# Kernel tuning notes

Hardware: AMD Instinct MI355X
Metric: run time of the kernel (lower is better)

The kernel has to match this reference:

```python
import jax, jax.numpy as jnp
import numpy as np

B, M, N, D, H = 8, 64, 64, 256, 8

def setup_inputs() -> dict:
    key = jax.random.key(0)
    kx, kq, kk, kv, ko = jax.random.split(key, 5)
    x = jax.random.normal(kx, (B, M, N, D), dtype=jnp.float32)
    q = jax.random.normal(kq, (H, D, D), dtype=jnp.float32)
    k = jax.random.normal(kk, (D, D), dtype=jnp.float32)
    v = jax.random.normal(kv, (D, D), dtype=jnp.float32)
    o = jax.random.normal(ko, (H, D, D), dtype=jnp.float32)
    return {"x": x, "q": q, "k": k, "v": v, "o": o}

def reference(x, q, k, v, o):
    # x: [b,m,n,d]; q,o: [h,d,d]; k,v: [d,d]
    Q = jnp.einsum('bmnd,hdk->bhmnk', x, q)      # [b,h,m,n,d]
    h_half = Q.shape[1] // 2
    Q1, Q2 = Q[:, :h_half], Q[:, h_half:]
    K = jnp.einsum('bmnd,dk->bmnk', x, k)        # [b,m,n,d]
    V = jnp.einsum('bmnd,dv->bmnv', x, v)        # [b,m,n,d]

    # Axis 1: attend along the m (row) axis for each column y
    logits1 = jnp.einsum('bhxyk,bzyk->bhyxz', Q1, K)   # [b,h/2,n,m,m]
    scores1 = jax.nn.softmax(logits1, axis=-1)
    O1 = jnp.einsum('bhyxz,bzyv->bhxyv', scores1, V)   # [b,h/2,m,n,d]

    # Axis 2: attend along the n (column) axis for each row x
    logits2 = jnp.einsum('bhxyk,bxzk->bhxyz', Q2, K)   # [b,h/2,m,n,n]
    scores2 = jax.nn.softmax(logits2, axis=-1)
    O2 = jnp.einsum('bhxyz,bxzv->bhxyv', scores2, V)   # [b,h/2,m,n,d]

    O = jnp.concatenate([O1, O2], axis=1)              # [b,h,m,n,d]
    # Faithful to original: 'bhmnd,hdv->bmnd' keeps d, sums over h and v
    Z = jnp.einsum('bhmnd,hdv->bmnd', O, o)
    return Z
```

## Files before the change

kernel.cpp:

```cpp
#include <hip/hip_runtime.h>

typedef unsigned short u16;
typedef __attribute__((ext_vector_type(8))) short short8;
typedef __attribute__((ext_vector_type(4))) float f32x4;

__device__ __forceinline__ float bf2f(u16 u){ return __uint_as_float(((unsigned)u)<<16); }
__device__ __forceinline__ u16 f2bf(float f){
  unsigned u = __float_as_uint(f);
  unsigned r = u + 0x7fffu + ((u>>16)&1u);
  return (u16)(r>>16);
}

#define MFMA16(a,b,c) __builtin_amdgcn_mfma_f32_16x16x32_bf16(a,b,c,0,0,0)

static constexpr int XS_STR  = 264;
static constexpr int PS_STR  = 72;
static constexpr int WT_STR  = 72;
static constexpr int XHI_OFF = 0;
static constexpr int XLO_OFF = 16896;
static constexpr int GT_OFF  = 33792;
static constexpr int XVT_OFF = 50688;
static constexpr int PS_OFF  = 69120;
static constexpr int SMRE_OFF= 73728;
static constexpr int SMEM_BYTES = (73728 + 512)*2;

static constexpr int MH_SMEM = 70656*2;


__global__ void prep_kernel(const float* __restrict__ k, const float* __restrict__ v,
                            const float* __restrict__ o, u16* __restrict__ khi,
                            u16* __restrict__ klo, u16* __restrict__ vT,
                            float* __restrict__ soP){
  __shared__ float Ts[64*65];
  const int blk = blockIdx.x, tid = threadIdx.x;
  if (blk < 64){
    int base = blk*1024 + tid*4;
    const float4 f4 = *(const float4*)(k + base);
    ushort4 hv, lv;
    hv.x=f2bf(f4.x); lv.x=f2bf(f4.x-bf2f(hv.x));
    hv.y=f2bf(f4.y); lv.y=f2bf(f4.y-bf2f(hv.y));
    hv.z=f2bf(f4.z); lv.z=f2bf(f4.z-bf2f(hv.z));
    hv.w=f2bf(f4.w); lv.w=f2bf(f4.w-bf2f(hv.w));
    *(ushort4*)&khi[base] = hv;
    *(ushort4*)&klo[base] = lv;
  } else if (blk < 80){
    int t = blk - 64;
    const int bi = (t>>2)<<6, bj = (t&3)<<6;
    #pragma unroll
    for (int p=0;p<4;p++){
      int idx4 = tid + (p<<8);
      int i = idx4 >> 4, c4 = (idx4 & 15) << 2;
      const float4 f4 = *(const float4*)(v + ((bi+i)<<8) + bj + c4);
      Ts[i*65+c4]=f4.x; Ts[i*65+c4+1]=f4.y; Ts[i*65+c4+2]=f4.z; Ts[i*65+c4+3]=f4.w;
    }
    __syncthreads();
    #pragma unroll
    for (int p=0;p<2;p++){
      int ch = tid + (p<<8);
      int j = ch >> 3, i8 = (ch & 7) << 3;
      short8 t8;
      #pragma unroll
      for (int e=0;e<8;e++) t8[e] = (short)f2bf(Ts[(i8+e)*65 + j]);
      *(short8*)&vT[((bj+j)<<8) + bi + i8] = t8;
    }
  } else {
    int p = blk - 80;
    int h = p >> 5, base = (p & 31) << 3;
    int w = tid >> 6, l = tid & 63;
    #pragma unroll
    for (int i=0;i<2;i++){
      int row = base + w*2 + i;
      const float4 f4 = *(const float4*)(o + (((h<<8)+row)<<8) + (l<<2));
      float s = f4.x + f4.y + f4.z + f4.w;
      #pragma unroll
      for (int off=32; off>=1; off>>=1) s += __shfl_xor(s, off, 64);
      if (l==0) soP[(h<<8)+row] = s;
    }
  }
}

__global__ __launch_bounds__(256,1) void mh_kernel(
    const float* __restrict__ q, const u16* __restrict__ khi,
    const u16* __restrict__ klo, u16* __restrict__ mhi, u16* __restrict__ mlo)
{
  extern __shared__ u16 sm[];
  u16* Qhi = sm;
  u16* Qlo = sm + 16896;
  u16* Chi = sm + 33792;
  u16* Clo = sm + 52224;

  const int tid = threadIdx.x;
  const int w = tid >> 6, lane = tid & 63;
  const int quad = lane >> 4, m16 = lane & 15;
  const int cw = w << 6, koq = quad << 3;
  const int h = blockIdx.x >> 2, dt = (blockIdx.x & 3) << 6;

  #pragma unroll
  for (int i=0;i<16;i++){
    int idx4 = i*256 + tid;
    int tr = idx4 >> 6, c4 = (idx4 & 63) << 2;
    const float4 xv = *(const float4*)(q + (((h<<8)+dt+tr)<<8) + c4);
    ushort4 hv, lv;
    hv.x=f2bf(xv.x); lv.x=f2bf(xv.x-bf2f(hv.x));
    hv.y=f2bf(xv.y); lv.y=f2bf(xv.y-bf2f(hv.y));
    hv.z=f2bf(xv.z); lv.z=f2bf(xv.z-bf2f(hv.z));
    hv.w=f2bf(xv.w); lv.w=f2bf(xv.w-bf2f(hv.w));
    *(ushort4*)&Qhi[tr*XS_STR + c4] = hv;
    *(ushort4*)&Qlo[tr*XS_STR + c4] = lv;
  }
  __syncthreads();

  const f32x4 zf = {0.f,0.f,0.f,0.f};
  f32x4 acc[4][4];
  #pragma unroll
  for (int r=0;r<4;r++)
    #pragma unroll
    for (int c=0;c<4;c++) acc[r][c] = zf;

  short8 Bh[2][4], Bl[2][4];
  #pragma unroll
  for (int c=0;c<4;c++){
    Bh[0][c] = *(const short8*)&khi[(cw + c*16 + m16)*256 + koq];
    Bl[0][c] = *(const short8*)&klo[(cw + c*16 + m16)*256 + koq];
  }
  #pragma unroll
  for (int kk=0;kk<8;kk++){
    const int cur = kk&1, nxt = cur^1;
    if (kk<7){
      const int ko2 = ((kk+1)<<5) + koq;
      #pragma unroll
      for (int c=0;c<4;c++){
        Bh[nxt][c] = *(const short8*)&khi[(cw + c*16 + m16)*256 + ko2];
        Bl[nxt][c] = *(const short8*)&klo[(cw + c*16 + m16)*256 + ko2];
      }
    }
    const int ko = (kk<<5) + koq;
    short8 Ah[4], Al[4];
    #pragma unroll
    for (int r=0;r<4;r++) Ah[r] = *(const short8*)&Qhi[(r*16+m16)*XS_STR + ko];
    #pragma unroll
    for (int r=0;r<4;r++) Al[r] = *(const short8*)&Qlo[(r*16+m16)*XS_STR + ko];
    #pragma unroll
    for (int r=0;r<4;r++)
      #pragma unroll
      for (int c=0;c<4;c++){
        acc[r][c] = MFMA16(Ah[r], Bh[cur][c], acc[r][c]);
        acc[r][c] = MFMA16(Ah[r], Bl[cur][c], acc[r][c]);
        acc[r][c] = MFMA16(Al[r], Bh[cur][c], acc[r][c]);
      }
  }

  #pragma unroll
  for (int r=0;r<4;r++)
    #pragma unroll
    for (int c=0;c<4;c++)
      #pragma unroll
      for (int g=0; g<4; g++){
        int drow = r*16 + quad*4 + g;
        int dp   = cw + c*16 + m16;
        float vv = acc[r][c][g];
        u16 hh = f2bf(vv);
        Chi[dp*WT_STR + drow] = hh;
        Clo[dp*WT_STR + drow] = f2bf(vv - bf2f(hh));
      }
  __syncthreads();

  #pragma unroll
  for (int p=0;p<8;p++){
    int ch = tid + (p<<8);
    int dp = ch >> 3, i8 = (ch & 7) << 3;
    *(int4*)&mhi[(((h<<8)+dp)<<8) + dt + i8] = *(const int4*)&Chi[dp*WT_STR + i8];
    *(int4*)&mlo[(((h<<8)+dp)<<8) + dt + i8] = *(const int4*)&Clo[dp*WT_STR + i8];
  }
}

__global__ __launch_bounds__(512,2) void attn_kernel(
    const float* __restrict__ x, const u16* __restrict__ mhiP,
    const u16* __restrict__ mloP, const u16* __restrict__ vT,
    const float* __restrict__ soP, float* __restrict__ out)
{
  extern __shared__ u16 sm[];
  u16* Xhi = sm + XHI_OFF;
  u16* Xlo = sm + XLO_OFF;
  u16* Gt  = sm + GT_OFF;
  u16* Xvt = sm + XVT_OFF;
  u16* Ps  = sm + PS_OFF;
  float* SMf = (float*)(sm + SMRE_OFF);

  const int tid  = threadIdx.x;
  const int w    = tid >> 6, lane = tid & 63;
  const int quad = lane >> 4, m16 = lane & 15;
  const int br   = blockIdx.x >> 9;
  const int idx  = blockIdx.x & 511;
  const int b    = idx >> 6, s = idx & 63;
  const int cw   = w << 5;
  const int rs   = (w >> 1) << 4;
  const int zh   = w & 1;
  const int koq  = quad << 3;

  auto tok = [&](int t)->int {
    int m = br ? s : t;
    int n = br ? t : s;
    return (((b<<6) + m) << 14) + (n << 8);
  };

  #pragma unroll
  for (int i=0;i<8;i++){
    int idx4 = i*512 + tid;
    int tr = idx4 >> 6, c4 = (idx4 & 63) << 2;
    const float4 xv = *(const float4*)(x + tok(tr) + c4);
    ushort4 hv, lv;
    hv.x=f2bf(xv.x); lv.x=f2bf(xv.x-bf2f(hv.x));
    hv.y=f2bf(xv.y); lv.y=f2bf(xv.y-bf2f(hv.y));
    hv.z=f2bf(xv.z); lv.z=f2bf(xv.z-bf2f(hv.z));
    hv.w=f2bf(xv.w); lv.w=f2bf(xv.w-bf2f(hv.w));
    *(ushort4*)&Xhi[tr*XS_STR + c4] = hv;
    *(ushort4*)&Xlo[tr*XS_STR + c4] = lv;
  }
  __syncthreads();

  const f32x4 zf = {0.f,0.f,0.f,0.f};
  f32x4 acc[4][2];

  auto mm3 = [&](const u16* __restrict__ Whi, const u16* __restrict__ Wlo){
    #pragma unroll
    for (int r=0;r<4;r++){ acc[r][0] = zf; acc[r][1] = zf; }
    short8 Bh[2][2], Bl[2][2];
    #pragma unroll
    for (int c=0;c<2;c++){
      Bh[0][c] = *(const short8*)&Whi[(cw + c*16 + m16)*256 + koq];
      Bl[0][c] = *(const short8*)&Wlo[(cw + c*16 + m16)*256 + koq];
    }
    #pragma unroll
    for (int kk=0;kk<8;kk++){
      const int cur = kk&1, nxt = cur^1;
      if (kk<7){
        const int ko2 = ((kk+1)<<5) + koq;
        #pragma unroll
        for (int c=0;c<2;c++){
          Bh[nxt][c] = *(const short8*)&Whi[(cw + c*16 + m16)*256 + ko2];
          Bl[nxt][c] = *(const short8*)&Wlo[(cw + c*16 + m16)*256 + ko2];
        }
      }
      const int ko = (kk<<5) + koq;
      short8 Ah[4], Al[4];
      #pragma unroll
      for (int r=0;r<4;r++) Ah[r] = *(const short8*)&Xhi[(r*16+m16)*XS_STR + ko];
      #pragma unroll
      for (int r=0;r<4;r++) Al[r] = *(const short8*)&Xlo[(r*16+m16)*XS_STR + ko];
      #pragma unroll
      for (int r=0;r<4;r++)
        #pragma unroll
        for (int c=0;c<2;c++){
          acc[r][c] = MFMA16(Ah[r], Bh[cur][c], acc[r][c]);
          acc[r][c] = MFMA16(Ah[r], Bl[cur][c], acc[r][c]);
          acc[r][c] = MFMA16(Al[r], Bh[cur][c], acc[r][c]);
        }
    }
  };

  {
    #pragma unroll
    for (int r=0;r<4;r++){ acc[r][0] = zf; acc[r][1] = zf; }
    #pragma unroll
    for (int kk=0;kk<8;kk++){
      const int ko = (kk<<5) + koq;
      short8 A[4], Bf[2];
      #pragma unroll
      for (int r=0;r<4;r++) A[r]  = *(const short8*)&Xhi[(r*16+m16)*XS_STR + ko];
      #pragma unroll
      for (int c=0;c<2;c++) Bf[c] = *(const short8*)&vT[(cw + c*16 + m16)*256 + ko];
      #pragma unroll
      for (int r=0;r<4;r++)
        #pragma unroll
        for (int c=0;c<2;c++) acc[r][c] = MFMA16(A[r], Bf[c], acc[r][c]);
    }
    #pragma unroll
    for (int r=0;r<4;r++)
      #pragma unroll
      for (int c=0;c<2;c++)
        #pragma unroll
        for (int g=0; g<4; g++){
          int z  = r*16 + quad*4 + g;
          int vc = cw + c*16 + m16;
          Xvt[vc*WT_STR + z] = f2bf(acc[r][c][g]);
        }
  }

  f32x4 Z[4][2];
  #pragma unroll
  for (int r=0;r<4;r++){ Z[r][0] = zf; Z[r][1] = zf; }

  for (int h=0; h<4; h++){
    const int gh = br*4 + h;

    mm3(mhiP + gh*65536, mloP + gh*65536);
    #pragma unroll
    for (int r=0;r<4;r++)
      #pragma unroll
      for (int c=0;c<2;c++)
        #pragma unroll
        for (int g=0; g<4; g++){
          int row = r*16 + quad*4 + g;
          int col = cw + c*16 + m16;
          Gt[row*XS_STR + col] = f2bf(acc[r][c][g]);
        }
    __syncthreads();

    f32x4 L[2];
    L[0] = zf; L[1] = zf;
    #pragma unroll
    for (int kk=0;kk<8;kk++){
      const int ko = (kk<<5) + koq;
      short8 A = *(const short8*)&Gt[(rs+m16)*XS_STR + ko];
      #pragma unroll
      for (int c=0;c<2;c++)
        L[c] = MFMA16(A, *(const short8*)&Xhi[((zh<<5) + c*16+m16)*XS_STR + ko], L[c]);
      #pragma unroll
      for (int c=0;c<2;c++)
        L[c] = MFMA16(A, *(const short8*)&Xlo[((zh<<5) + c*16+m16)*XS_STR + ko], L[c]);
    }
    __syncthreads();
    #pragma unroll
    for (int r=0;r<4;r++)
      #pragma unroll
      for (int c=0;c<2;c++)
        #pragma unroll
        for (int g=0; g<4; g++){
          int row = r*16 + quad*4 + g;
          int col = cw + c*16 + m16;
          float vv = acc[r][c][g];
          u16 hh = f2bf(vv);
          Gt[row*XS_STR + col] = f2bf(vv - bf2f(hh));
        }
    __syncthreads();

    #pragma unroll
    for (int kk=0;kk<8;kk++){
      const int ko = (kk<<5) + koq;
      short8 A = *(const short8*)&Gt[(rs+m16)*XS_STR + ko];
      #pragma unroll
      for (int c=0;c<2;c++)
        L[c] = MFMA16(A, *(const short8*)&Xhi[((zh<<5) + c*16+m16)*XS_STR + ko], L[c]);
    }

    float mxl[4], sml[4];
    #pragma unroll
    for (int g=0; g<4; g++){
      float mx = fmaxf(L[0][g], L[1][g]);
      #pragma unroll
      for (int off=1; off<16; off<<=1) mx = fmaxf(mx, __shfl_xor(mx, off, 64));
      float sum = 0.f;
      #pragma unroll
      for (int c=0;c<2;c++){ float e = __expf(L[c][g]-mx); L[c][g] = e; sum += e; }
      #pragma unroll
      for (int off=1; off<16; off<<=1) sum += __shfl_xor(sum, off, 64);
      mxl[g] = mx; sml[g] = sum;
      if (m16 == 0){
        int row = rs + quad*4 + g;
        SMf[row*4 + zh*2]     = mx;
        SMf[row*4 + zh*2 + 1] = sum;
      }
    }
    __syncthreads();
    #pragma unroll
    for (int g=0; g<4; g++){
      int row = rs + quad*4 + g;
      float mxo = SMf[row*4 + (zh^1)*2];
      float smo = SMf[row*4 + (zh^1)*2 + 1];
      float M   = fmaxf(mxl[g], mxo);
      float al  = __expf(mxl[g]-M), ao = __expf(mxo-M);
      float scale = al / (sml[g]*al + smo*ao);
      #pragma unroll
      for (int c=0;c<2;c++)
        Ps[row*PS_STR + (zh<<5) + c*16 + m16] = f2bf(L[c][g]*scale);
    }
    __syncthreads();

    #pragma unroll
    for (int r=0;r<4;r++){ acc[r][0] = zf; acc[r][1] = zf; }
    #pragma unroll
    for (int kk=0;kk<2;kk++){
      const int ko = (kk<<5) + koq;
      short8 A[4], Bf[2];
      #pragma unroll
      for (int r=0;r<4;r++) A[r]  = *(const short8*)&Ps[(r*16+m16)*PS_STR + ko];
      #pragma unroll
      for (int c=0;c<2;c++) Bf[c] = *(const short8*)&Xvt[(cw + c*16 + m16)*WT_STR + ko];
      #pragma unroll
      for (int r=0;r<4;r++)
        #pragma unroll
        for (int c=0;c<2;c++) acc[r][c] = MFMA16(A[r], Bf[c], acc[r][c]);
    }
    float sc[2];
    sc[0] = soP[gh*256 + cw + m16];
    sc[1] = soP[gh*256 + cw + 16 + m16];
    #pragma unroll
    for (int r=0;r<4;r++)
      #pragma unroll
      for (int c=0;c<2;c++)
        #pragma unroll
        for (int g=0; g<4; g++) Z[r][c][g] += sc[c]*acc[r][c][g];
  }

  #pragma unroll
  for (int r=0;r<4;r++)
    #pragma unroll
    for (int c=0;c<2;c++)
      #pragma unroll
      for (int g=0; g<4; g++){
        int t   = r*16 + quad*4 + g;
        int col = cw + c*16 + m16;
        atomicAdd(&out[tok(t) + col], Z[r][c][g]);
      }
}

extern "C" void kernel_launch(void* const* d_in, const int* in_sizes, int n_in,
                              void* d_out, int out_size, void* d_ws, size_t ws_size,
                              hipStream_t stream) {
  const float* x = (const float*)d_in[0];
  const float* q = (const float*)d_in[1];
  const float* k = (const float*)d_in[2];
  const float* v = (const float*)d_in[3];
  const float* o = (const float*)d_in[4];
  u16* ws   = (u16*)d_ws;
  u16* mhi  = ws;
  u16* mlo  = ws + 524288;
  u16* khi  = ws + 1048576;
  u16* klo  = ws + 1114112;
  u16* vT   = ws + 1179648;
  float* soP = (float*)(ws + 1245184);
  float* out = (float*)d_out;

  (void)hipMemsetAsync(d_out, 0, (size_t)out_size*sizeof(float), stream);
  prep_kernel<<<336, 256, 0, stream>>>(k, v, o, khi, klo, vT, soP);
  (void)hipFuncSetAttribute(reinterpret_cast<const void*>(&mh_kernel),
                            hipFuncAttributeMaxDynamicSharedMemorySize, MH_SMEM);
  mh_kernel<<<32, 256, MH_SMEM, stream>>>(q, khi, klo, mhi, mlo);

  (void)hipFuncSetAttribute(reinterpret_cast<const void*>(&attn_kernel),
                            hipFuncAttributeMaxDynamicSharedMemorySize, SMEM_BYTES);
  attn_kernel<<<1024, 512, SMEM_BYTES, stream>>>(x, mhi, mlo, vT, soP, out);
}
```

Before: 355.1 us.

## Retile attention warps to 2x4 fragments, cache X-hi fragments in registers, fold memset into prep

Warp tiling in the attention kernel changes from 4 row-tiles by 2 column-tiles to 2 row-tiles by 4 column-tiles. Each warp now loads fewer X fragments from LDS and more weight fragments from global memory per MFMA step. The Xhi B-fragments used in the logits GEMMs are preloaded into 16 registers and reused across all heads. The output memset is moved into extra prep_kernel blocks, and the manual double-buffering of global weight loads is removed in favour of straight per-step loads. This raises register pressure and exposes global-load latency that was previously hidden by prefetch.

```diff
diff --git a/kernel.cpp b/kernel.cpp
--- a/kernel.cpp
+++ b/kernel.cpp
@@ -30,7 +30,7 @@
 __global__ void prep_kernel(const float* __restrict__ k, const float* __restrict__ v,
                             const float* __restrict__ o, u16* __restrict__ khi,
                             u16* __restrict__ klo, u16* __restrict__ vT,
-                            float* __restrict__ soP){
+                            float* __restrict__ soP, float4* __restrict__ outz){
   __shared__ float Ts[64*65];
   const int blk = blockIdx.x, tid = threadIdx.x;
   if (blk < 64){
@@ -63,7 +63,7 @@
       for (int e=0;e<8;e++) t8[e] = (short)f2bf(Ts[(i8+e)*65 + j]);
       *(short8*)&vT[((bj+j)<<8) + bi + i8] = t8;
     }
-  } else {
+  } else if (blk < 336){
     int p = blk - 80;
     int h = p >> 5, base = (p & 31) << 3;
     int w = tid >> 6, l = tid & 63;
@@ -76,6 +76,11 @@
       for (int off=32; off>=1; off>>=1) s += __shfl_xor(s, off, 64);
       if (l==0) soP[(h<<8)+row] = s;
     }
+  } else {
+    int z = blk - 336;
+    const float4 zf4 = {0.f,0.f,0.f,0.f};
+    #pragma unroll
+    for (int i=0;i<16;i++) outz[z*4096 + i*256 + tid] = zf4;
   }
 }
 
@@ -117,36 +122,26 @@
     #pragma unroll
     for (int c=0;c<4;c++) acc[r][c] = zf;
 
-  short8 Bh[2][4], Bl[2][4];
-  #pragma unroll
-  for (int c=0;c<4;c++){
-    Bh[0][c] = *(const short8*)&khi[(cw + c*16 + m16)*256 + koq];
-    Bl[0][c] = *(const short8*)&klo[(cw + c*16 + m16)*256 + koq];
-  }
   #pragma unroll
   for (int kk=0;kk<8;kk++){
-    const int cur = kk&1, nxt = cur^1;
-    if (kk<7){
-      const int ko2 = ((kk+1)<<5) + koq;
+    const int ko = (kk<<5) + koq;
+    short8 Ah[4], Al[4], Bh[4], Bl[4];
+    #pragma unroll
+    for (int c=0;c<4;c++){
+      Bh[c] = *(const short8*)&khi[(cw + c*16 + m16)*256 + ko];
+      Bl[c] = *(const short8*)&klo[(cw + c*16 + m16)*256 + ko];
+    }
+    #pragma unroll
+    for (int r=0;r<4;r++) Ah[r] = *(const short8*)&Qhi[(r*16+m16)*XS_STR + ko];
+    #pragma unroll
+    for (int r=0;r<4;r++) Al[r] = *(const short8*)&Qlo[(r*16+m16)*XS_STR + ko];
+    #pragma unroll
+    for (int r=0;r<4;r++)
       #pragma unroll
       for (int c=0;c<4;c++){
-        Bh[nxt][c] = *(const short8*)&khi[(cw + c*16 + m16)*256 + ko2];
-        Bl[nxt][c] = *(const short8*)&klo[(cw + c*16 + m16)*256 + ko2];
-      }
-    }
-    const int ko = (kk<<5) + koq;
-    short8 Ah[4], Al[4];
-    #pragma unroll
-    for (int r=0;r<4;r++) Ah[r] = *(const short8*)&Qhi[(r*16+m16)*XS_STR + ko];
-    #pragma unroll
-    for (int r=0;r<4;r++) Al[r] = *(const short8*)&Qlo[(r*16+m16)*XS_STR + ko];
-    #pragma unroll
-    for (int r=0;r<4;r++)
-      #pragma unroll
-      for (int c=0;c<4;c++){
-        acc[r][c] = MFMA16(Ah[r], Bh[cur][c], acc[r][c]);
-        acc[r][c] = MFMA16(Ah[r], Bl[cur][c], acc[r][c]);
-        acc[r][c] = MFMA16(Al[r], Bh[cur][c], acc[r][c]);
+        acc[r][c] = MFMA16(Ah[r], Bh[c], acc[r][c]);
+        acc[r][c] = MFMA16(Ah[r], Bl[c], acc[r][c]);
+        acc[r][c] = MFMA16(Al[r], Bh[c], acc[r][c]);
       }
   }
 
@@ -193,7 +188,8 @@
   const int br   = blockIdx.x >> 9;
   const int idx  = blockIdx.x & 511;
   const int b    = idx >> 6, s = idx & 63;
-  const int cw   = w << 5;
+  const int rtb  = (w & 1) << 1;
+  const int cwb  = (w >> 1) << 6;
   const int rs   = (w >> 1) << 4;
   const int zh   = w & 1;
   const int koq  = quad << 3;
@@ -219,90 +215,94 @@
   }
   __syncthreads();
 
+  short8 XB[16];
+  #pragma unroll
+  for (int kk=0;kk<8;kk++)
+    #pragma unroll
+    for (int c=0;c<2;c++)
+      XB[kk*2+c] = *(const short8*)&Xhi[((zh<<5) + c*16 + m16)*XS_STR + (kk<<5) + koq];
+
   const f32x4 zf = {0.f,0.f,0.f,0.f};
-  f32x4 acc[4][2];
+  f32x4 acc[2][4];
 
   auto mm3 = [&](const u16* __restrict__ Whi, const u16* __restrict__ Wlo){
     #pragma unroll
-    for (int r=0;r<4;r++){ acc[r][0] = zf; acc[r][1] = zf; }
-    short8 Bh[2][2], Bl[2][2];
-    #pragma unroll
-    for (int c=0;c<2;c++){
-      Bh[0][c] = *(const short8*)&Whi[(cw + c*16 + m16)*256 + koq];
-      Bl[0][c] = *(const short8*)&Wlo[(cw + c*16 + m16)*256 + koq];
-    }
-    #pragma unroll
-    for (int kk=0;kk<8;kk++){
-      const int cur = kk&1, nxt = cur^1;
-      if (kk<7){
-        const int ko2 = ((kk+1)<<5) + koq;
-        #pragma unroll
-        for (int c=0;c<2;c++){
-          Bh[nxt][c] = *(const short8*)&Whi[(cw + c*16 + m16)*256 + ko2];
-          Bl[nxt][c] = *(const short8*)&Wlo[(cw + c*16 + m16)*256 + ko2];
-        }
-      }
-      const int ko = (kk<<5) + koq;
-      short8 Ah[4], Al[4];
-      #pragma unroll
-      for (int r=0;r<4;r++) Ah[r] = *(const short8*)&Xhi[(r*16+m16)*XS_STR + ko];
-      #pragma unroll
-      for (int r=0;r<4;r++) Al[r] = *(const short8*)&Xlo[(r*16+m16)*XS_STR + ko];
-      #pragma unroll
-      for (int r=0;r<4;r++)
-        #pragma unroll
-        for (int c=0;c<2;c++){
-          acc[r][c] = MFMA16(Ah[r], Bh[cur][c], acc[r][c]);
-          acc[r][c] = MFMA16(Ah[r], Bl[cur][c], acc[r][c]);
-          acc[r][c] = MFMA16(Al[r], Bh[cur][c], acc[r][c]);
-        }
-    }
-  };
-
-  {
-    #pragma unroll
-    for (int r=0;r<4;r++){ acc[r][0] = zf; acc[r][1] = zf; }
+    for (int r=0;r<2;r++)
+      #pragma unroll
+      for (int c=0;c<4;c++) acc[r][c] = zf;
     #pragma unroll
     for (int kk=0;kk<8;kk++){
       const int ko = (kk<<5) + koq;
-      short8 A[4], Bf[2];
-      #pragma unroll
-      for (int r=0;r<4;r++) A[r]  = *(const short8*)&Xhi[(r*16+m16)*XS_STR + ko];
-      #pragma unroll
-      for (int c=0;c<2;c++) Bf[c] = *(const short8*)&vT[(cw + c*16 + m16)*256 + ko];
-      #pragma unroll
-      for (int r=0;r<4;r++)
-        #pragma unroll
-        for (int c=0;c<2;c++) acc[r][c] = MFMA16(A[r], Bf[c], acc[r][c]);
-    }
-    #pragma unroll
-    for (int r=0;r<4;r++)
-      #pragma unroll
-      for (int c=0;c<2;c++)
+      short8 Ah[2], Al[2], Bh[4], Bl[4];
+      #pragma unroll
+      for (int c=0;c<4;c++){
+        Bh[c] = *(const short8*)&Whi[(cwb + c*16 + m16)*256 + ko];
+        Bl[c] = *(const short8*)&Wlo[(cwb + c*16 + m16)*256 + ko];
+      }
+      #pragma unroll
+      for (int r=0;r<2;r++){
+        Ah[r] = *(const short8*)&Xhi[((rtb+r)*16+m16)*XS_STR + ko];
+        Al[r] = *(const short8*)&Xlo[((rtb+r)*16+m16)*XS_STR + ko];
+      }
+      #pragma unroll
+      for (int r=0;r<2;r++)
+        #pragma unroll
+        for (int c=0;c<4;c++){
+          acc[r][c] = MFMA16(Ah[r], Bh[c], acc[r][c]);
+          acc[r][c] = MFMA16(Ah[r], Bl[c], acc[r][c]);
+          acc[r][c] = MFMA16(Al[r], Bh[c], acc[r][c]);
+        }
+    }
+  };
+
+  {
+    #pragma unroll
+    for (int r=0;r<2;r++)
+      #pragma unroll
+      for (int c=0;c<4;c++) acc[r][c] = zf;
+    #pragma unroll
+    for (int kk=0;kk<8;kk++){
+      const int ko = (kk<<5) + koq;
+      short8 A[2], Bf[4];
+      #pragma unroll
+      for (int c=0;c<4;c++) Bf[c] = *(const short8*)&vT[(cwb + c*16 + m16)*256 + ko];
+      #pragma unroll
+      for (int r=0;r<2;r++) A[r] = *(const short8*)&Xhi[((rtb+r)*16+m16)*XS_STR + ko];
+      #pragma unroll
+      for (int r=0;r<2;r++)
+        #pragma unroll
+        for (int c=0;c<4;c++) acc[r][c] = MFMA16(A[r], Bf[c], acc[r][c]);
+    }
+    #pragma unroll
+    for (int r=0;r<2;r++)
+      #pragma unroll
+      for (int c=0;c<4;c++)
         #pragma unroll
         for (int g=0; g<4; g++){
-          int z  = r*16 + quad*4 + g;
-          int vc = cw + c*16 + m16;
+          int z  = (rtb+r)*16 + quad*4 + g;
+          int vc = cwb + c*16 + m16;
           Xvt[vc*WT_STR + z] = f2bf(acc[r][c][g]);
         }
   }
 
-  f32x4 Z[4][2];
-  #pragma unroll
-  for (int r=0;r<4;r++){ Z[r][0] = zf; Z[r][1] = zf; }
+  f32x4 Z[2][4];
+  #pragma unroll
+  for (int r=0;r<2;r++)
+    #pragma unroll
+    for (int c=0;c<4;c++) Z[r][c] = zf;
 
   for (int h=0; h<4; h++){
     const int gh = br*4 + h;
 
     mm3(mhiP + gh*65536, mloP + gh*65536);
     #pragma unroll
-    for (int r=0;r<4;r++)
-      #pragma unroll
-      for (int c=0;c<2;c++)
+    for (int r=0;r<2;r++)
+      #pragma unroll
+      for (int c=0;c<4;c++)
         #pragma unroll
         for (int g=0; g<4; g++){
-          int row = r*16 + quad*4 + g;
-          int col = cw + c*16 + m16;
+          int row = (rtb+r)*16 + quad*4 + g;
+          int col = cwb + c*16 + m16;
           Gt[row*XS_STR + col] = f2bf(acc[r][c][g]);
         }
     __syncthreads();
@@ -314,21 +314,21 @@
       const int ko = (kk<<5) + koq;
       short8 A = *(const short8*)&Gt[(rs+m16)*XS_STR + ko];
       #pragma unroll
-      for (int c=0;c<2;c++)
-        L[c] = MFMA16(A, *(const short8*)&Xhi[((zh<<5) + c*16+m16)*XS_STR + ko], L[c]);
-      #pragma unroll
-      for (int c=0;c<2;c++)
-        L[c] = MFMA16(A, *(const short8*)&Xlo[((zh<<5) + c*16+m16)*XS_STR + ko], L[c]);
-    }
-    __syncthreads();
-    #pragma unroll
-    for (int r=0;r<4;r++)
-      #pragma unroll
-      for (int c=0;c<2;c++)
+      for (int c=0;c<2;c++){
+        L[c] = MFMA16(A, XB[kk*2+c], L[c]);
+        short8 Bl = *(const short8*)&Xlo[((zh<<5) + c*16 + m16)*XS_STR + ko];
+        L[c] = MFMA16(A, Bl, L[c]);
+      }
+    }
+    __syncthreads();
+    #pragma unroll
+    for (int r=0;r<2;r++)
+      #pragma unroll
+      for (int c=0;c<4;c++)
         #pragma unroll
         for (int g=0; g<4; g++){
-          int row = r*16 + quad*4 + g;
-          int col = cw + c*16 + m16;
+          int row = (rtb+r)*16 + quad*4 + g;
+          int col = cwb + c*16 + m16;
           float vv = acc[r][c][g];
           u16 hh = f2bf(vv);
           Gt[row*XS_STR + col] = f2bf(vv - bf2f(hh));
@@ -341,7 +341,7 @@
       short8 A = *(const short8*)&Gt[(rs+m16)*XS_STR + ko];
       #pragma unroll
       for (int c=0;c<2;c++)
-        L[c] = MFMA16(A, *(const short8*)&Xhi[((zh<<5) + c*16+m16)*XS_STR + ko], L[c]);
+        L[c] = MFMA16(A, XB[kk*2+c], L[c]);
     }
 
     float mxl[4], sml[4];
@@ -378,39 +378,41 @@
     __syncthreads();
 
     #pragma unroll
-    for (int r=0;r<4;r++){ acc[r][0] = zf; acc[r][1] = zf; }
+    for (int r=0;r<2;r++)
+      #pragma unroll
+      for (int c=0;c<4;c++) acc[r][c] = zf;
     #pragma unroll
     for (int kk=0;kk<2;kk++){
       const int ko = (kk<<5) + koq;
-      short8 A[4], Bf[2];
-      #pragma unroll
-      for (int r=0;r<4;r++) A[r]  = *(const short8*)&Ps[(r*16+m16)*PS_STR + ko];
-      #pragma unroll
-      for (int c=0;c<2;c++) Bf[c] = *(const short8*)&Xvt[(cw + c*16 + m16)*WT_STR + ko];
-      #pragma unroll
-      for (int r=0;r<4;r++)
-        #pragma unroll
-        for (int c=0;c<2;c++) acc[r][c] = MFMA16(A[r], Bf[c], acc[r][c]);
-    }
-    float sc[2];
-    sc[0] = soP[gh*256 + cw + m16];
-    sc[1] = soP[gh*256 + cw + 16 + m16];
-    #pragma unroll
-    for (int r=0;r<4;r++)
-      #pragma unroll
-      for (int c=0;c<2;c++)
+      short8 A[2], Bf[4];
+      #pragma unroll
+      for (int c=0;c<4;c++) Bf[c] = *(const short8*)&Xvt[(cwb + c*16 + m16)*WT_STR + ko];
+      #pragma unroll
+      for (int r=0;r<2;r++) A[r] = *(const short8*)&Ps[((rtb+r)*16+m16)*PS_STR + ko];
+      #pragma unroll
+      for (int r=0;r<2;r++)
+        #pragma unroll
+        for (int c=0;c<4;c++) acc[r][c] = MFMA16(A[r], Bf[c], acc[r][c]);
+    }
+    float sc[4];
+    #pragma unroll
+    for (int c=0;c<4;c++) sc[c] = soP[gh*256 + cwb + c*16 + m16];
+    #pragma unroll
+    for (int r=0;r<2;r++)
+      #pragma unroll
+      for (int c=0;c<4;c++)
         #pragma unroll
         for (int g=0; g<4; g++) Z[r][c][g] += sc[c]*acc[r][c][g];
   }
 
   #pragma unroll
-  for (int r=0;r<4;r++)
-    #pragma unroll
-    for (int c=0;c<2;c++)
+  for (int r=0;r<2;r++)
+    #pragma unroll
+    for (int c=0;c<4;c++)
       #pragma unroll
       for (int g=0; g<4; g++){
-        int t   = r*16 + quad*4 + g;
-        int col = cw + c*16 + m16;
+        int t   = (rtb+r)*16 + quad*4 + g;
+        int col = cwb + c*16 + m16;
         atomicAdd(&out[tok(t) + col], Z[r][c][g]);
       }
 }
@@ -432,8 +434,7 @@
   float* soP = (float*)(ws + 1245184);
   float* out = (float*)d_out;
 
-  (void)hipMemsetAsync(d_out, 0, (size_t)out_size*sizeof(float), stream);
-  prep_kernel<<<336, 256, 0, stream>>>(k, v, o, khi, klo, vT, soP);
+  prep_kernel<<<848, 256, 0, stream>>>(k, v, o, khi, klo, vT, soP, (float4*)d_out);
   (void)hipFuncSetAttribute(reinterpret_cast<const void*>(&mh_kernel),
                             hipFuncAttributeMaxDynamicSharedMemorySize, MH_SMEM);
   mh_kernel<<<32, 256, MH_SMEM, stream>>>(q, khi, klo, mhi, mlo);
```

New measurement: 559.9 us. 57.7% more time.
